# Kernel optimization log

Measured on AMD Instinct MI355X. Metric: run time of the kernel, lower is better.

The kernel has to match this reference:

```python
import jax, jax.numpy as jnp
import numpy as np

D_MODEL = 768
N_HEADS = 12
D_FF = 3072
EPS = 1e-5


def layer_norm(x, gamma, beta):
    mu = jnp.mean(x, axis=-1, keepdims=True)
    var = jnp.mean(jnp.square(x - mu), axis=-1, keepdims=True)
    return (x - mu) * jax.lax.rsqrt(var + EPS) * gamma + beta


def setup_inputs() -> dict:
    key = jax.random.key(0)
    ks = jax.random.split(key, 8)
    s = 1.0 / np.sqrt(D_MODEL)
    sf = 1.0 / np.sqrt(D_FF)
    return {
        "x": jax.random.normal(ks[0], (2, 2048, D_MODEL), dtype=jnp.float32),
        "w_qkv": jax.random.uniform(ks[1], (D_MODEL, 3 * D_MODEL), jnp.float32, -s, s),
        "b_qkv": jnp.zeros((3 * D_MODEL,), jnp.float32),
        "w_out": jax.random.uniform(ks[2], (D_MODEL, D_MODEL), jnp.float32, -s, s),
        "b_out": jnp.zeros((D_MODEL,), jnp.float32),
        "w1": jax.random.uniform(ks[3], (D_MODEL, D_FF), jnp.float32, -s, s),
        "b1": jnp.zeros((D_FF,), jnp.float32),
        "w2": jax.random.uniform(ks[4], (D_FF, D_MODEL), jnp.float32, -sf, sf),
        "b2": jnp.zeros((D_MODEL,), jnp.float32),
        "g1": jnp.ones((D_MODEL,), jnp.float32),
        "be1": jnp.zeros((D_MODEL,), jnp.float32),
        "g2": jnp.ones((D_MODEL,), jnp.float32),
        "be2": jnp.zeros((D_MODEL,), jnp.float32),
    }


def reference(x, w_qkv, b_qkv, w_out, b_out, w1, b1, w2, b2, g1, be1, g2, be2):
    B, S, D = x.shape
    H = N_HEADS
    dk = D // H
    qkv = x @ w_qkv + b_qkv                      # [B,S,3D]
    q, k, v = jnp.split(qkv, 3, axis=-1)
    # [B,H,S,dk]
    q = q.reshape(B, S, H, dk).transpose(0, 2, 1, 3)
    k = k.reshape(B, S, H, dk).transpose(0, 2, 1, 3)
    v = v.reshape(B, S, H, dk).transpose(0, 2, 1, 3)
    scores = jnp.einsum('bhqd,bhkd->bhqk', q, k) / np.sqrt(dk)  # [B,H,S,S]
    attn = jax.nn.softmax(scores, axis=-1)
    o = jnp.einsum('bhqk,bhkd->bhqd', attn, v)
    o = o.transpose(0, 2, 1, 3).reshape(B, S, D)
    attn_out = o @ w_out + b_out
    x = layer_norm(x + attn_out, g1, be1)
    ffn = jax.nn.gelu(x @ w1 + b1, approximate=False) @ w2 + b2
    return layer_norm(x + ffn, g2, be2)
```

## Files before the change

kernel.cpp:

```cpp
#include <hip/hip_runtime.h>
#include <hip/hip_bf16.h>
#include <math.h>

#define D_MODEL 768
#define NH 12
#define DFF 3072
#define BB 2
#define SS 2048
#define MM (BB*SS)
#define DK 64

typedef _Float16 half8 __attribute__((ext_vector_type(8)));
typedef _Float16 half4 __attribute__((ext_vector_type(4)));
typedef float f32x4 __attribute__((ext_vector_type(4)));

template<int AM, int EPI>
__launch_bounds__(256)
__global__ void hgemm_k(const _Float16* __restrict__ A,
                        const _Float16* __restrict__ Bt,
                        const float* __restrict__ bias,
                        float* __restrict__ Cf, _Float16* __restrict__ Ch,
                        int M, int N, int K,
                        _Float16* __restrict__ qo, _Float16* __restrict__ ko,
                        _Float16* __restrict__ vo)
{
    constexpr int BM = AM * 32;
    constexpr int NA = BM / 8;
    constexpr int NI = NA + 16;
    __shared__ _Float16 Als[2][BM * 64];
    __shared__ _Float16 Bls[2][128 * 64];

    const int tid  = threadIdx.x;
    const int wv   = tid >> 6, lane = tid & 63;
    const int l15  = lane & 15, lg = lane >> 4;
    const int wr   = wv >> 1,  wc = wv & 1;
    const int m0   = blockIdx.y * BM, n0 = blockIdx.x * 128;

    f32x4 acc[AM][4];
    #pragma unroll
    for (int m = 0; m < AM; m++)
        #pragma unroll
        for (int n = 0; n < 4; n++)
            acc[m][n][0] = acc[m][n][1] = acc[m][n][2] = acc[m][n][3] = 0.0f;

    const char* Ab = (const char*)A;
    const char* Bb = (const char*)Bt;

#define GSTAGE(buf, kt)                                                       \
    {                                                                         \
        _Pragma("unroll")                                                     \
        for (int inst = wv; inst < NI; inst += 4) {                           \
            const bool isA = inst < NA;                                       \
            const int  li  = isA ? inst : inst - NA;                          \
            const int  p   = li * 1024 + lane * 16;                           \
            const int  lo  = p ^ (((p >> 7) & 7) << 4);                       \
            const int  row = lo >> 7, kb = lo & 127;                          \
            const char* src = isA                                             \
                ? Ab + ((size_t)(m0 + row) * K + (kt)) * 2 + kb               \
                : Bb + ((size_t)(n0 + row) * K + (kt)) * 2 + kb;              \
            char* dst = (isA ? (char*)Als[buf] : (char*)Bls[buf]) + li * 1024;\
            __builtin_amdgcn_global_load_lds(                                 \
                (const __attribute__((address_space(1))) void*)src,           \
                (__attribute__((address_space(3))) void*)dst, 16, 0, 0);      \
        }                                                                     \
    }

    GSTAGE(0, 0);
    asm volatile("s_waitcnt vmcnt(0)" ::: "memory");
    __syncthreads();

    const int nt = K >> 6;
    for (int it = 0; it < nt; ++it) {
        const int cur = it & 1;
        if (it + 1 < nt) GSTAGE(cur ^ 1, (it + 1) << 6);

        const char* Al = (const char*)Als[cur];
        const char* Bl = (const char*)Bls[cur];

        __builtin_amdgcn_s_setprio(1);
        #pragma unroll
        for (int ks = 0; ks < 2; ks++) {
            half8 af[AM], bf[4];
            #pragma unroll
            for (int m = 0; m < AM; m++) {
                int row = wr * (AM * 16) + m * 16 + l15;
                int off = (row * 128 + ks * 64 + lg * 16) ^ ((row & 7) << 4);
                af[m] = *(const half8*)(Al + off);
            }
            #pragma unroll
            for (int n = 0; n < 4; n++) {
                int row = wc * 64 + n * 16 + l15;
                int off = (row * 128 + ks * 64 + lg * 16) ^ ((row & 7) << 4);
                bf[n] = *(const half8*)(Bl + off);
            }
            #pragma unroll
            for (int m = 0; m < AM; m++)
                #pragma unroll
                for (int n = 0; n < 4; n++)
                    acc[m][n] = __builtin_amdgcn_mfma_f32_16x16x32_f16(
                        af[m], bf[n], acc[m][n], 0, 0, 0);
        }
        __builtin_amdgcn_s_setprio(0);

        asm volatile("s_waitcnt vmcnt(0)" ::: "memory");
        __syncthreads();
    }
#undef GSTAGE

    #pragma unroll
    for (int m = 0; m < AM; m++) {
        #pragma unroll
        for (int n = 0; n < 4; n++) {
            int col = n0 + wc * 64 + n * 16 + l15;
            float bs = bias[col];
            #pragma unroll
            for (int r = 0; r < 4; r++) {
                int row = m0 + wr * (AM * 16) + m * 16 + lg * 4 + r;
                float val = acc[m][n][r] + bs;
                if (EPI == 0) {
                    Cf[(size_t)row * N + col] = val;
                } else if (EPI == 1) {
                    val = 0.5f * val * (1.0f + erff(val * 0.70710678118654752f));
                    Ch[(size_t)row * N + col] = (_Float16)val;
                } else {
                    int which = col / D_MODEL;
                    int c = col - which * D_MODEL;
                    int hh = c >> 6, dd = c & 63;
                    int bq = row >> 11, si = row & 2047;
                    _Float16 hv = (_Float16)val;
                    if (which == 0)
                        qo[((((size_t)bq * NH + hh) * SS) + si) * DK + dd] = hv;
                    else if (which == 1)
                        ko[((((size_t)bq * NH + hh) * SS) + si) * DK + dd] = hv;
                    else
                        vo[(((size_t)bq * NH + hh) * DK + dd) * SS + si] = hv;
                }
            }
        }
    }
}

__launch_bounds__(256)
__global__ void attn_mfma_k(const _Float16* __restrict__ Q,
                            const _Float16* __restrict__ K,
                            const _Float16* __restrict__ VT,
                            _Float16* __restrict__ O)
{
    __shared__ _Float16 Kls[2][64 * 64];
    __shared__ _Float16 Vls[2][64 * 64];
    __shared__ _Float16 Pl[4 * 1024];

    const int tid  = threadIdx.x;
    const int wv   = tid >> 6;
    const int lane = tid & 63;
    const int l15  = lane & 15;
    const int lg   = lane >> 4;

    const int bh = blockIdx.y;
    const int b  = bh / NH, h = bh - b * NH;
    const int q0 = blockIdx.x * 64 + wv * 16;

    const _Float16* Qb = Q + (size_t)bh * SS * DK;
    const char* Kb = (const char*)(K  + (size_t)bh * SS * DK);
    const char* Vb = (const char*)(VT + (size_t)bh * DK * SS);

#define ATTN_STAGE(buf, kt)                                                   \
    {                                                                         \
        _Pragma("unroll")                                                     \
        for (int w = 0; w < 4; w++) {                                         \
            int inst = wv + w * 4;                                            \
            bool isK = inst < 8;                                              \
            int li = isK ? inst : inst - 8;                                   \
            int p  = li * 1024 + lane * 16;                                   \
            int lo = p ^ (((p >> 7) & 7) << 4);                               \
            int row = lo >> 7, kbyte = lo & 127;                              \
            const char* src = isK                                             \
                ? (Kb + (size_t)((kt) + row) * 128 + kbyte)                   \
                : (Vb + (size_t)row * (SS * 2) + (size_t)(kt) * 2 + kbyte);   \
            char* dst = (isK ? (char*)Kls[buf] : (char*)Vls[buf]) + li * 1024;\
            __builtin_amdgcn_global_load_lds(                                 \
                (const __attribute__((address_space(1))) void*)src,           \
                (__attribute__((address_space(3))) void*)dst, 16, 0, 0);      \
        }                                                                     \
    }

    ATTN_STAGE(0, 0);

    half8 qa0 = *(const half8*)&Qb[(size_t)(q0 + l15) * DK + lg * 8];
    half8 qa1 = *(const half8*)&Qb[(size_t)(q0 + l15) * DK + 32 + lg * 8];
    #pragma unroll
    for (int i = 0; i < 8; i++) {
        qa0[i] = qa0[i] * (_Float16)0.18033688f;
        qa1[i] = qa1[i] * (_Float16)0.18033688f;
    }

    f32x4 po[4];
    float m_[4], l_[4];
    #pragma unroll
    for (int r = 0; r < 4; r++) {
        po[r][0] = po[r][1] = po[r][2] = po[r][3] = 0.0f;
        m_[r] = -1e30f; l_[r] = 0.0f;
    }

    char* Pw = (char*)&Pl[wv * 1024];
    const int prd = (l15 * 128 + lg * 16) ^ ((l15 & 7) << 4);

    asm volatile("s_waitcnt vmcnt(0)" ::: "memory");
    __syncthreads();

    for (int it = 0; it < SS / 64; ++it) {
        const int cur = it & 1;
        if (it + 1 < SS / 64) ATTN_STAGE(cur ^ 1, (it + 1) * 64);

        const char* Kc = (const char*)Kls[cur];
        const char* Vc = (const char*)Vls[cur];

        f32x4 sc[4];
        __builtin_amdgcn_s_setprio(1);
        #pragma unroll
        for (int t = 0; t < 4; t++) {
            int row = t * 16 + l15;
            int off0 = (row * 128 + lg * 16) ^ ((row & 7) << 4);
            int off1 = (row * 128 + 64 + lg * 16) ^ ((row & 7) << 4);
            half8 kb0 = *(const half8*)(Kc + off0);
            half8 kb1 = *(const half8*)(Kc + off1);
            f32x4 z;
            z[0] = z[1] = z[2] = z[3] = 0.0f;
            z = __builtin_amdgcn_mfma_f32_16x16x32_f16(qa0, kb0, z, 0, 0, 0);
            sc[t] = __builtin_amdgcn_mfma_f32_16x16x32_f16(qa1, kb1, z, 0, 0, 0);
        }
        __builtin_amdgcn_s_setprio(0);

        float rmv[4];
        float need = 0.0f;
        #pragma unroll
        for (int r = 0; r < 4; r++) {
            float rm = fmaxf(fmaxf(sc[0][r], sc[1][r]), fmaxf(sc[2][r], sc[3][r]));
            rm = fmaxf(rm, __shfl_xor(rm, 1));
            rm = fmaxf(rm, __shfl_xor(rm, 2));
            rm = fmaxf(rm, __shfl_xor(rm, 4));
            rm = fmaxf(rm, __shfl_xor(rm, 8));
            rmv[r] = rm;
            need = fmaxf(need, rm - m_[r]);
        }
        if (!__all(need <= 11.5f)) {
            #pragma unroll
            for (int r = 0; r < 4; r++) {
                float mn = fmaxf(m_[r], rmv[r]);
                float alpha = exp2f(m_[r] - mn);
                m_[r] = mn;
                l_[r] *= alpha;
                #pragma unroll
                for (int dt = 0; dt < 4; dt++) po[dt][r] *= alpha;
            }
        }
        #pragma unroll
        for (int r = 0; r < 4; r++) {
            float rs = 0.0f;
            #pragma unroll
            for (int t = 0; t < 4; t++) {
                float p = exp2f(sc[t][r] - m_[r]);
                sc[t][r] = p;
                rs += p;
            }
            rs += __shfl_xor(rs, 1);
            rs += __shfl_xor(rs, 2);
            rs += __shfl_xor(rs, 4);
            rs += __shfl_xor(rs, 8);
            l_[r] += rs;
        }

        #pragma unroll
        for (int t = 0; t < 4; t++)
            #pragma unroll
            for (int r = 0; r < 4; r++) {
                int row = lg * 4 + r, col = t * 16 + l15;
                int off = (row * 128 + col * 2) ^ ((row & 7) << 4);
                *(_Float16*)(Pw + off) = (_Float16)sc[t][r];
            }
        asm volatile("s_waitcnt lgkmcnt(0)" ::: "memory");
        __builtin_amdgcn_sched_barrier(0);

        half8 pa0 = *(const half8*)(Pw + prd);
        half8 pa1 = *(const half8*)(Pw + (prd ^ 64));

        __builtin_amdgcn_s_setprio(1);
        #pragma unroll
        for (int dt = 0; dt < 4; dt++) {
            int row = dt * 16 + l15;
            int off0 = (row * 128 + lg * 16) ^ ((row & 7) << 4);
            int off1 = (row * 128 + 64 + lg * 16) ^ ((row & 7) << 4);
            half8 vb0 = *(const half8*)(Vc + off0);
            half8 vb1 = *(const half8*)(Vc + off1);
            po[dt] = __builtin_amdgcn_mfma_f32_16x16x32_f16(pa0, vb0, po[dt], 0, 0, 0);
            po[dt] = __builtin_amdgcn_mfma_f32_16x16x32_f16(pa1, vb1, po[dt], 0, 0, 0);
        }
        __builtin_amdgcn_s_setprio(0);

        asm volatile("s_waitcnt vmcnt(0)" ::: "memory");
        __syncthreads();
    }
#undef ATTN_STAGE

    #pragma unroll
    for (int r = 0; r < 4; r++) {
        float inv = 1.0f / l_[r];
        int qrow = q0 + lg * 4 + r;
        size_t base = (size_t)(b * SS + qrow) * D_MODEL + h * DK;
        #pragma unroll
        for (int dt = 0; dt < 4; dt++)
            O[base + dt * 16 + l15] = (_Float16)(po[dt][r] * inv);
    }
}

template<bool RH, bool OH>
__launch_bounds__(256)
__global__ void ln_k(const void* __restrict__ xres, const float* __restrict__ y,
                     const float* __restrict__ gamma, const float* __restrict__ beta,
                     void* __restrict__ outp)
{
    const int row  = blockIdx.x * 4 + (threadIdx.x >> 6);
    const int lane = threadIdx.x & 63;
    const size_t base = (size_t)row * D_MODEL;

    float v[12];
    float sum = 0.0f, ssq = 0.0f;
    #pragma unroll
    for (int ch = 0; ch < 3; ch++) {
        int col = ch * 256 + lane * 4;
        float4 yv = *(const float4*)&y[base + col];
        float xr[4];
        if (RH) {
            half4 hv = *(const half4*)((const _Float16*)xres + base + col);
            #pragma unroll
            for (int i = 0; i < 4; i++) xr[i] = (float)hv[i];
        } else {
            float4 xv = *(const float4*)((const float*)xres + base + col);
            xr[0] = xv.x; xr[1] = xv.y; xr[2] = xv.z; xr[3] = xv.w;
        }
        float yy[4] = {yv.x, yv.y, yv.z, yv.w};
        #pragma unroll
        for (int i = 0; i < 4; i++) {
            float t = xr[i] + yy[i];
            v[ch * 4 + i] = t;
            sum += t;
            ssq += t * t;
        }
    }
    #pragma unroll
    for (int msk = 32; msk >= 1; msk >>= 1) {
        sum += __shfl_xor(sum, msk);
        ssq += __shfl_xor(ssq, msk);
    }

    const float mu  = sum * (1.0f / D_MODEL);
    const float var = ssq * (1.0f / D_MODEL) - mu * mu;
    const float inv = rsqrtf(var + 1e-5f);

    #pragma unroll
    for (int ch = 0; ch < 3; ch++) {
        int col = ch * 256 + lane * 4;
        float4 gv = *(const float4*)&gamma[col];
        float4 bv = *(const float4*)&beta[col];
        float g[4] = {gv.x, gv.y, gv.z, gv.w};
        float be[4] = {bv.x, bv.y, bv.z, bv.w};
        if (OH) {
            half4 o;
            #pragma unroll
            for (int i = 0; i < 4; i++)
                o[i] = (_Float16)((v[ch * 4 + i] - mu) * inv * g[i] + be[i]);
            *(half4*)((_Float16*)outp + base + col) = o;
        } else {
            float4 o;
            o.x = (v[ch * 4 + 0] - mu) * inv * g[0] + be[0];
            o.y = (v[ch * 4 + 1] - mu) * inv * g[1] + be[1];
            o.z = (v[ch * 4 + 2] - mu) * inv * g[2] + be[2];
            o.w = (v[ch * 4 + 3] - mu) * inv * g[3] + be[3];
            *(float4*)((float*)outp + base + col) = o;
        }
    }
}

__launch_bounds__(256)
__global__ void castx_k(const float* __restrict__ in, _Float16* __restrict__ out,
                        int n8)
{
    int i = blockIdx.x * 256 + threadIdx.x;
    if (i < n8) {
        float4 a = ((const float4*)in)[2 * i];
        float4 b = ((const float4*)in)[2 * i + 1];
        half8 h = {(_Float16)a.x, (_Float16)a.y, (_Float16)a.z, (_Float16)a.w,
                   (_Float16)b.x, (_Float16)b.y, (_Float16)b.z, (_Float16)b.w};
        ((half8*)out)[i] = h;
    }
}

__launch_bounds__(256)
__global__ void wcast_k(const float* __restrict__ src, _Float16* __restrict__ dst,
                        int K, int N)
{
    __shared__ float t[32][33];
    const int k0 = blockIdx.y * 32, n0 = blockIdx.x * 32;
    const int c = threadIdx.x & 31, r8 = threadIdx.x >> 5;
    #pragma unroll
    for (int rr = 0; rr < 4; rr++) {
        int r = rr * 8 + r8;
        t[r][c] = src[(size_t)(k0 + r) * N + n0 + c];
    }
    __syncthreads();
    #pragma unroll
    for (int rr = 0; rr < 4; rr++) {
        int n = rr * 8 + r8;
        dst[(size_t)(n0 + n) * K + k0 + c] = (_Float16)t[c][n];
    }
}

extern "C" void kernel_launch(void* const* d_in, const int* in_sizes, int n_in,
                              void* d_out, int out_size, void* d_ws, size_t ws_size,
                              hipStream_t stream)
{
    const float* x     = (const float*)d_in[0];
    const float* w_qkv = (const float*)d_in[1];
    const float* b_qkv = (const float*)d_in[2];
    const float* w_out = (const float*)d_in[3];
    const float* b_out = (const float*)d_in[4];
    const float* w1    = (const float*)d_in[5];
    const float* b1    = (const float*)d_in[6];
    const float* w2    = (const float*)d_in[7];
    const float* b2    = (const float*)d_in[8];
    const float* g1    = (const float*)d_in[9];
    const float* be1   = (const float*)d_in[10];
    const float* g2    = (const float*)d_in[11];
    const float* be2   = (const float*)d_in[12];

    char* w = (char*)d_ws;
    _Float16* q        = (_Float16*)(w);
    _Float16* kk       = (_Float16*)(w + 6291456);
    _Float16* vv       = (_Float16*)(w + 12582912);
    _Float16* ffn_h    = (_Float16*)(w);
    _Float16* xh       = (_Float16*)(w + 25165824);
    _Float16* attn_oh  = (_Float16*)(w + 25165824);
    _Float16* wqkvT    = (_Float16*)(w + 31457280);
    _Float16* woutT    = (_Float16*)(w + 34996224);
    _Float16* w1T      = (_Float16*)(w + 36175872);
    _Float16* w2T      = (_Float16*)(w + 40894464);
    float*    attn_proj= (float*)(w + 45613056);
    float*    ffn_out  = (float*)(w + 45613056);
    _Float16* x1h      = (_Float16*)(w + 58195968);
    float* out = (float*)d_out;

    dim3 blk(256);

    castx_k<<<(MM * D_MODEL / 8 + 255) / 256, blk, 0, stream>>>(x, xh, MM * D_MODEL / 8);
    wcast_k<<<dim3(2304 / 32, 768 / 32), blk, 0, stream>>>(w_qkv, wqkvT, 768, 2304);
    wcast_k<<<dim3(768 / 32, 768 / 32), blk, 0, stream>>>(w_out, woutT, 768, 768);
    wcast_k<<<dim3(3072 / 32, 768 / 32), blk, 0, stream>>>(w1, w1T, 768, 3072);
    wcast_k<<<dim3(768 / 32, 3072 / 32), blk, 0, stream>>>(w2, w2T, 3072, 768);

    hgemm_k<4, 2><<<dim3(2304 / 128, MM / 128), blk, 0, stream>>>(
        xh, wqkvT, b_qkv, nullptr, nullptr, MM, 2304, D_MODEL, q, kk, vv);

    attn_mfma_k<<<dim3(SS / 64, BB * NH), blk, 0, stream>>>(q, kk, vv, attn_oh);

    hgemm_k<2, 0><<<dim3(768 / 128, MM / 64), blk, 0, stream>>>(
        attn_oh, woutT, b_out, attn_proj, nullptr, MM, D_MODEL, D_MODEL,
        nullptr, nullptr, nullptr);

    ln_k<false, true><<<MM / 4, blk, 0, stream>>>(x, attn_proj, g1, be1, x1h);

    hgemm_k<4, 1><<<dim3(DFF / 128, MM / 128), blk, 0, stream>>>(
        x1h, w1T, b1, nullptr, ffn_h, MM, DFF, D_MODEL, nullptr, nullptr, nullptr);

    hgemm_k<2, 0><<<dim3(768 / 128, MM / 64), blk, 0, stream>>>(
        ffn_h, w2T, b2, ffn_out, nullptr, MM, D_MODEL, DFF, nullptr, nullptr, nullptr);

    ln_k<true, false><<<MM / 4, blk, 0, stream>>>(x1h, ffn_out, g2, be2, out);
}
```

Before: 352.2 us.

## Use tanh GELU approximation and compute softmax row sums with MFMA

Replaces the erf-based GELU in the FFN epilogue with a tanh approximation built from a fast exp and a hardware reciprocal. In attention, the Q scale drops the log2e factor and uses __expf instead of exp2f, with the rescale threshold adjusted to match. The per-row sum of probabilities no longer uses shuffle reductions; it comes from two extra MFMAs of P against a ones vector. This removes shuffle and erf cost but changes GELU numerics to an approximation and adds MFMA work per tile. __expf may also lower to exp2 plus a multiply.

```diff
diff --git a/kernel.cpp b/kernel.cpp
--- a/kernel.cpp
+++ b/kernel.cpp
@@ -120,7 +120,12 @@
                 if (EPI == 0) {
                     Cf[(size_t)row * N + col] = val;
                 } else if (EPI == 1) {
-                    val = 0.5f * val * (1.0f + erff(val * 0.70710678118654752f));
+                    float xx = val;
+                    float u = xx * fmaf(0.044715f * xx, xx, 1.0f);
+                    u = fminf(fmaxf(u, -9.0f), 9.0f);
+                    float t = __expf(1.5957691f * u);
+                    float th = (t - 1.0f) * __builtin_amdgcn_rcpf(t + 1.0f);
+                    val = 0.5f * xx * (1.0f + th);
                     Ch[(size_t)row * N + col] = (_Float16)val;
                 } else {
                     int which = col / D_MODEL;
@@ -190,9 +195,13 @@
     half8 qa1 = *(const half8*)&Qb[(size_t)(q0 + l15) * DK + 32 + lg * 8];
     #pragma unroll
     for (int i = 0; i < 8; i++) {
-        qa0[i] = qa0[i] * (_Float16)0.18033688f;
-        qa1[i] = qa1[i] * (_Float16)0.18033688f;
-    }
+        qa0[i] = qa0[i] * (_Float16)0.125f;
+        qa1[i] = qa1[i] * (_Float16)0.125f;
+    }
+
+    const half8 ones = {(_Float16)1.0f, (_Float16)1.0f, (_Float16)1.0f,
+                        (_Float16)1.0f, (_Float16)1.0f, (_Float16)1.0f,
+                        (_Float16)1.0f, (_Float16)1.0f};
 
     f32x4 po[4];
     float m_[4], l_[4];
@@ -243,11 +252,11 @@
             rmv[r] = rm;
             need = fmaxf(need, rm - m_[r]);
         }
-        if (!__all(need <= 11.5f)) {
+        if (!__all(need <= 8.0f)) {
             #pragma unroll
             for (int r = 0; r < 4; r++) {
                 float mn = fmaxf(m_[r], rmv[r]);
-                float alpha = exp2f(m_[r] - mn);
+                float alpha = __expf(m_[r] - mn);
                 m_[r] = mn;
                 l_[r] *= alpha;
                 #pragma unroll
@@ -255,20 +264,10 @@
             }
         }
         #pragma unroll
-        for (int r = 0; r < 4; r++) {
-            float rs = 0.0f;
-            #pragma unroll
-            for (int t = 0; t < 4; t++) {
-                float p = exp2f(sc[t][r] - m_[r]);
-                sc[t][r] = p;
-                rs += p;
-            }
-            rs += __shfl_xor(rs, 1);
-            rs += __shfl_xor(rs, 2);
-            rs += __shfl_xor(rs, 4);
-            rs += __shfl_xor(rs, 8);
-            l_[r] += rs;
-        }
+        for (int r = 0; r < 4; r++)
+            #pragma unroll
+            for (int t = 0; t < 4; t++)
+                sc[t][r] = __expf(sc[t][r] - m_[r]);
 
         #pragma unroll
         for (int t = 0; t < 4; t++)
@@ -285,6 +284,15 @@
         half8 pa1 = *(const half8*)(Pw + (prd ^ 64));
 
         __builtin_amdgcn_s_setprio(1);
+        {
+            f32x4 lz;
+            lz[0] = lz[1] = lz[2] = lz[3] = 0.0f;
+            lz = __builtin_amdgcn_mfma_f32_16x16x32_f16(pa0, ones, lz, 0, 0, 0);
+            lz = __builtin_amdgcn_mfma_f32_16x16x32_f16(pa1, ones, lz, 0, 0, 0);
+            #pragma unroll
+            for (int r = 0; r < 4; r++) l_[r] += lz[r];
+        }
+
         #pragma unroll
         for (int dt = 0; dt < 4; dt++) {
             int row = dt * 16 + l15;
```

Result: faster. 325.4 us (-7.6%).
